# Kernel optimization log

Measured on AMD Instinct MI355X. Metric: run time of the kernel, lower is better.

Reference implementation:

```python
import jax, jax.numpy as jnp
import numpy as np

N, E = 50000, 800000
IN_CH, H, OUT_CH, ED, L = 64, 128, 128, 1, 4


def setup_inputs() -> dict:
    key = jax.random.key(0)
    ks = jax.random.split(key, 24)
    s = 0.02
    inp = {
        'h': jax.random.normal(ks[0], (N, IN_CH), jnp.float32),
        'coords': jax.random.normal(ks[1], (N, 3), jnp.float32),
        'edge_attr': jax.random.normal(ks[2], (E, ED), jnp.float32),
        'emb_in_W': jax.random.normal(ks[3], (IN_CH, H), jnp.float32) * s,
        'emb_in_b': jnp.zeros((H,), jnp.float32),
        'emb_out_W': jax.random.normal(ks[4], (H, OUT_CH), jnp.float32) * s,
        'emb_out_b': jnp.zeros((OUT_CH,), jnp.float32),
        # per-layer stacked params
        'eW1': jax.random.normal(ks[5], (L, 2 * H + 1 + ED, H), jnp.float32) * s,
        'eb1': jnp.zeros((L, H), jnp.float32),
        'eW2': jax.random.normal(ks[6], (L, H, H), jnp.float32) * s,
        'eb2': jnp.zeros((L, H), jnp.float32),
        'cW1': jax.random.normal(ks[7], (L, H, H), jnp.float32) * s,
        'cb1': jnp.zeros((L, H), jnp.float32),
        'cWc': jax.random.normal(ks[8], (L, H, 1), jnp.float32) * 0.001,  # xavier gain=0.001, no bias
        'nW1': jax.random.normal(ks[9], (L, 2 * H, H), jnp.float32) * s,
        'nb1': jnp.zeros((L, H), jnp.float32),
        'nW2': jax.random.normal(ks[10], (L, H, H), jnp.float32) * s,
        'nb2': jnp.zeros((L, H), jnp.float32),
        'edge_index': jax.random.randint(ks[11], (2, E), 0, N, jnp.int32),
    }
    return inp


def _egnn_forward(h, coords, edge_attr, emb_in_W, emb_in_b, emb_out_W, emb_out_b,
                  eW1, eb1, eW2, eb2, cW1, cb1, cWc, nW1, nb1, nW2, nb2, edge_index):
    silu = jax.nn.silu
    row, col = edge_index[0], edge_index[1]  # PyG: j=source=row, i=target=col
    # count of incoming edges per target node, for coords_agg='mean'
    counts = jax.ops.segment_sum(jnp.ones((E,), jnp.float32), col, num_segments=N)
    counts = jnp.maximum(counts, 1.0)[:, None]
    h = h @ emb_in_W + emb_in_b
    for l in range(L):
        coord_diff = coords[row] - coords[col]                       # [E,3]
        dist = jnp.sum(coord_diff * coord_diff, axis=-1, keepdims=True)  # [E,1]
        # message: edge MLP on cat(x_i, x_j, dist, edge_attr)
        edge_in = jnp.concatenate([h[col], h[row], dist, edge_attr], axis=-1)
        ef = silu(edge_in @ eW1[l] + eb1[l])
        ef = silu(ef @ eW2[l] + eb2[l])                               # [E,H]
        cw = silu(ef @ cW1[l] + cb1[l]) @ cWc[l]                      # [E,1]
        coord_upd = coord_diff * cw                                   # [E,3]
        # aggregate to target nodes
        agg_feat = jax.ops.segment_sum(ef, col, num_segments=N)       # [N,H]
        agg_coord = jax.ops.segment_sum(coord_upd, col, num_segments=N) / counts
        # node update (residual)
        node_in = jnp.concatenate([h, agg_feat], axis=-1)
        upd = silu(node_in @ nW1[l] + nb1[l]) @ nW2[l] + nb2[l]
        h = h + upd
        coords = coords + agg_coord
    h = h @ emb_out_W + emb_out_b
    return h, coords


def reference(h, coords, edge_attr, emb_in_W, emb_in_b, emb_out_W, emb_out_b,
              eW1, eb1, eW2, eb2, cW1, cb1, cWc, nW1, nb1, nW2, nb2, edge_index):
    return _egnn_forward(h, coords, edge_attr, emb_in_W, emb_in_b, emb_out_W, emb_out_b,
                         eW1, eb1, eW2, eb2, cW1, cb1, cWc, nW1, nb1, nW2, nb2, edge_index)
```

## Files before the change

kernel.cpp:

```cpp
#include <hip/hip_runtime.h>

constexpr int Nn = 50000;
constexpr int Ee = 800000;
constexpr int EF_STR  = 136;
constexpr int NIN_STR = 264;
constexpr int HIN_STR = 72;
constexpr int NB_SCAN = (Nn + 255) / 256;

typedef short s8v __attribute__((ext_vector_type(8)));
typedef float f4v __attribute__((ext_vector_type(4)));

__device__ __forceinline__ ushort f2bf(float f) {
    uint u = __float_as_uint(f);
    uint r = (u + 0x7FFFu + ((u >> 16) & 1u)) >> 16;
    return (ushort)r;
}
__device__ __forceinline__ ushort f2bf_t(float f) {
    return (ushort)(__float_as_uint(f) >> 16);
}
__device__ __forceinline__ float bf2f(ushort s) {
    return __uint_as_float(((uint)s) << 16);
}
__device__ __forceinline__ float silu_f(float x) {
    return x * __fdividef(1.0f, 1.0f + __expf(-x));
}
__device__ __forceinline__ uint pack2bf_t(float lo, float hi) {
    return __builtin_amdgcn_perm(__float_as_uint(hi), __float_as_uint(lo), 0x07060302u);
}
__device__ __forceinline__ uint pack2bf_r(float lo, float hi) {
    uint a = __float_as_uint(lo) + 0x8000u;
    uint b = __float_as_uint(hi) + 0x8000u;
    return __builtin_amdgcn_perm(b, a, 0x07060302u);
}

__device__ __forceinline__ void swz_one(const float* src, ushort* dst, int K, int lstride, int KC, int idx)
{
    int per = KC * 4096;
    int l = idx / per, r = idx % per;
    int fb = r >> 9, rem = r & 511;
    int lane = rem >> 3, jj = rem & 7;
    int kc = fb >> 3, t = fb & 7;
    int k = kc * 32 + ((lane >> 4) << 3) + jj;
    int n = t * 16 + (lane & 15);
    float v = (k < K) ? src[(size_t)l * lstride + (size_t)k * 128 + n] : 0.0f;
    dst[idx] = f2bf(v);
}
__global__ void __launch_bounds__(256) k_swz_all(
    const float* __restrict__ eW1, const float* __restrict__ eW2, const float* __restrict__ cW1,
    const float* __restrict__ nW1, const float* __restrict__ nW2,
    const float* __restrict__ inW, const float* __restrict__ outW,
    ushort* __restrict__ oT, ushort* __restrict__ oM,
    ushort* __restrict__ o2, ushort* __restrict__ o3,
    ushort* __restrict__ o4, ushort* __restrict__ o5,
    ushort* __restrict__ o6, ushort* __restrict__ o7)
{
    int gid = blockIdx.x * 256 + threadIdx.x;
    if (gid < 65536)       swz_one(eW1,         oT, 128, 33024, 4, gid);
    else if (gid < 131072) swz_one(eW1 + 16384, oM, 128, 33024, 4, gid - 65536);
    else if (gid < 196608) swz_one(eW2, o2, 128, 16384, 4, gid - 131072);
    else if (gid < 262144) swz_one(cW1, o3, 128, 16384, 4, gid - 196608);
    else if (gid < 393216) swz_one(nW1, o4, 256, 32768, 8, gid - 262144);
    else if (gid < 458752) swz_one(nW2, o5, 128, 16384, 4, gid - 393216);
    else if (gid < 466944) swz_one(inW, o6, 64, 8192, 2, gid - 458752);
    else if (gid < 483328) swz_one(outW, o7, 128, 16384, 4, gid - 466944);
}

__global__ void __launch_bounds__(256) k_count(const int* __restrict__ eidx, int* __restrict__ ecnt)
{
    int e = blockIdx.x * 256 + threadIdx.x;
    atomicAdd(&ecnt[eidx[Ee + e]], 1);
}

__global__ void __launch_bounds__(256) k_bsum(const int* __restrict__ ecnt, int* __restrict__ bsum)
{
    __shared__ int ws[4];
    int tid = threadIdx.x, lane = tid & 63, w = tid >> 6;
    int i = blockIdx.x * 256 + tid;
    int x = (i < Nn) ? ecnt[i] : 0;
    #pragma unroll
    for (int off = 1; off < 64; off <<= 1) x += __shfl_xor(x, off, 64);
    if (lane == 0) ws[w] = x;
    __syncthreads();
    if (tid == 0) bsum[blockIdx.x] = ws[0] + ws[1] + ws[2] + ws[3];
}
__global__ void __launch_bounds__(256) k_bscan(int* __restrict__ bsum)
{
    __shared__ int ws[4];
    int tid = threadIdx.x, lane = tid & 63, w = tid >> 6;
    int x = (tid < NB_SCAN) ? bsum[tid] : 0;
    int s = x;
    #pragma unroll
    for (int off = 1; off < 64; off <<= 1) {
        int t = __shfl_up(s, off, 64);
        if (lane >= off) s += t;
    }
    if (lane == 63) ws[w] = s;
    __syncthreads();
    if (tid == 0) { int a = 0; for (int k = 0; k < 4; k++) { int t = ws[k]; ws[k] = a; a += t; } }
    __syncthreads();
    int excl = ws[w] + s - x;
    if (tid < NB_SCAN) bsum[tid] = excl;
}
__global__ void __launch_bounds__(256) k_cursor(const int* __restrict__ ecnt,
                                               const int* __restrict__ boff, int* __restrict__ cursor)
{
    __shared__ int ws[4];
    int tid = threadIdx.x, lane = tid & 63, w = tid >> 6;
    int i = blockIdx.x * 256 + tid;
    int x = (i < Nn) ? ecnt[i] : 0;
    int s = x;
    #pragma unroll
    for (int off = 1; off < 64; off <<= 1) {
        int t = __shfl_up(s, off, 64);
        if (lane >= off) s += t;
    }
    if (lane == 63) ws[w] = s;
    __syncthreads();
    if (tid == 0) { int a = 0; for (int k = 0; k < 4; k++) { int t = ws[k]; ws[k] = a; a += t; } }
    __syncthreads();
    int excl = ws[w] + s - x + boff[blockIdx.x];
    if (i < Nn) cursor[i] = excl;
}

__global__ void __launch_bounds__(256) k_scatter(
    const int* __restrict__ eidx, const float* __restrict__ edge_attr,
    int* __restrict__ cursor,
    int* __restrict__ srow, int* __restrict__ scol, float* __restrict__ sattr)
{
    int e = blockIdx.x * 256 + threadIdx.x;
    int r = eidx[e], c = eidx[Ee + e];
    int p = atomicAdd(&cursor[c], 1);
    srow[p] = r; scol[p] = c; sattr[p] = edge_attr[e];
}

__global__ void __launch_bounds__(512, 2) k_emb(
    const float* __restrict__ h_in, const float* __restrict__ coords,
    const ushort* __restrict__ ws_, const float* __restrict__ b,
    float* __restrict__ hbuf, ushort* __restrict__ hbf, float* __restrict__ cbuf)
{
    __shared__ alignas(16) ushort s_h[64 * HIN_STR];
    const int tid = threadIdx.x;
    const int nb = blockIdx.x * 64;
    #pragma unroll
    for (int i = 0; i < 2; i++) {
        int idx = i * 512 + tid;
        int e = idx >> 4, ch = idx & 15;
        int node = nb + e;
        float4 f = make_float4(0.f, 0.f, 0.f, 0.f);
        if (node < Nn) f = *(const float4*)(h_in + (size_t)node * 64 + ch * 4);
        ushort4 u; u.x = f2bf(f.x); u.y = f2bf(f.y); u.z = f2bf(f.z); u.w = f2bf(f.w);
        *(ushort4*)(s_h + e * HIN_STR + ch * 4) = u;
    }
    if (tid < 192) {
        int n = nb + tid / 3, d = tid % 3;
        if (n < Nn) cbuf[n * 3 + d] = coords[n * 3 + d];
    }
    __syncthreads();
    const int lane = tid & 63, wave = tid >> 6;
    const int m = lane & 15, quad = lane >> 4;
    const int ws2 = wave >> 2, wt = wave & 3;
    const int rbase = ws2 * 32;
    f4v acc[2][2];
    #pragma unroll
    for (int nt = 0; nt < 2; nt++) { acc[nt][0] = (f4v){0,0,0,0}; acc[nt][1] = (f4v){0,0,0,0}; }
    const ushort* aBase = ws_ + wt * 1024 + lane * 8;
    #pragma unroll
    for (int kc = 0; kc < 2; kc++) {
        s8v a0 = *(const s8v*)(aBase + kc * 4096);
        s8v a1 = *(const s8v*)(aBase + kc * 4096 + 512);
        #pragma unroll
        for (int nt = 0; nt < 2; nt++) {
            s8v bf = *(const s8v*)(s_h + (rbase + nt * 16 + m) * HIN_STR + kc * 32 + quad * 8);
            acc[nt][0] = __builtin_amdgcn_mfma_f32_16x16x32_bf16(a0, bf, acc[nt][0], 0, 0, 0);
            acc[nt][1] = __builtin_amdgcn_mfma_f32_16x16x32_bf16(a1, bf, acc[nt][1], 0, 0, 0);
        }
    }
    #pragma unroll
    for (int nt = 0; nt < 2; nt++) {
        int node = nb + rbase + nt * 16 + m;
        if (node < Nn) {
            #pragma unroll
            for (int ct = 0; ct < 2; ct++) {
                int colb = (wt * 2 + ct) * 16 + quad * 4;
                float4 bb = *(const float4*)(b + colb);
                float v0 = acc[nt][ct][0] + bb.x;
                float v1 = acc[nt][ct][1] + bb.y;
                float v2 = acc[nt][ct][2] + bb.z;
                float v3 = acc[nt][ct][3] + bb.w;
                *(float4*)(hbuf + (size_t)node * 128 + colb) = make_float4(v0, v1, v2, v3);
                uint2 pk; pk.x = pack2bf_r(v0, v1); pk.y = pack2bf_r(v2, v3);
                *(uint2*)(hbf + (size_t)node * 128 + colb) = pk;
            }
        }
    }
}

__global__ void __launch_bounds__(512, 2) k_uv(
    const ushort* __restrict__ hbf,
    const ushort* __restrict__ topW, const ushort* __restrict__ midW,
    const float* __restrict__ b1, ushort* __restrict__ uvb)
{
    __shared__ alignas(16) ushort s_h[64 * EF_STR];
    const int tid = threadIdx.x;
    const int nb = blockIdx.x * 64;
    #pragma unroll
    for (int i = 0; i < 2; i++) {
        int idx = i * 512 + tid;
        int e = idx >> 4, ch = idx & 15;
        int node = nb + e;
        uint4 v = make_uint4(0, 0, 0, 0);
        if (node < Nn) v = *(const uint4*)(hbf + (size_t)node * 128 + ch * 8);
        *(uint4*)(s_h + e * EF_STR + ch * 8) = v;
    }
    __syncthreads();
    const int lane = tid & 63, wave = tid >> 6;
    const int m = lane & 15, quad = lane >> 4;
    const int ws2 = wave >> 2, wt = wave & 3;
    const int rbase = ws2 * 32;
    f4v au[2][2], av[2][2];
    #pragma unroll
    for (int ct = 0; ct < 2; ct++) {
        float4 bb = *(const float4*)(b1 + (wt * 2 + ct) * 16 + quad * 4);
        au[0][ct] = (f4v){bb.x, bb.y, bb.z, bb.w};
        au[1][ct] = au[0][ct];
        av[0][ct] = (f4v){0,0,0,0};
        av[1][ct] = (f4v){0,0,0,0};
    }
    const ushort* tBase = topW + wt * 1024 + (size_t)lane * 8;
    const ushort* mBase = midW + wt * 1024 + (size_t)lane * 8;
    #pragma unroll
    for (int kc = 0; kc < 4; kc++) {
        s8v t0 = *(const s8v*)(tBase + kc * 4096);
        s8v t1 = *(const s8v*)(tBase + kc * 4096 + 512);
        s8v m0 = *(const s8v*)(mBase + kc * 4096);
        s8v m1 = *(const s8v*)(mBase + kc * 4096 + 512);
        #pragma unroll
        for (int nt = 0; nt < 2; nt++) {
            s8v bf = *(const s8v*)(s_h + (rbase + nt * 16 + m) * EF_STR + kc * 32 + quad * 8);
            au[nt][0] = __builtin_amdgcn_mfma_f32_16x16x32_bf16(t0, bf, au[nt][0], 0, 0, 0);
            au[nt][1] = __builtin_amdgcn_mfma_f32_16x16x32_bf16(t1, bf, au[nt][1], 0, 0, 0);
            av[nt][0] = __builtin_amdgcn_mfma_f32_16x16x32_bf16(m0, bf, av[nt][0], 0, 0, 0);
            av[nt][1] = __builtin_amdgcn_mfma_f32_16x16x32_bf16(m1, bf, av[nt][1], 0, 0, 0);
        }
    }
    #pragma unroll
    for (int nt = 0; nt < 2; nt++) {
        int node = nb + rbase + nt * 16 + m;
        if (node < Nn) {
            #pragma unroll
            for (int ct = 0; ct < 2; ct++) {
                int colb = (wt * 2 + ct) * 16 + quad * 4;
                uint2 pu; pu.x = pack2bf_r(au[nt][ct][0], au[nt][ct][1]);
                          pu.y = pack2bf_r(au[nt][ct][2], au[nt][ct][3]);
                *(uint2*)(uvb + (size_t)node * 256 + colb) = pu;
                uint2 pv; pv.x = pack2bf_r(av[nt][ct][0], av[nt][ct][1]);
                          pv.y = pack2bf_r(av[nt][ct][2], av[nt][ct][3]);
                *(uint2*)(uvb + (size_t)node * 256 + 128 + colb) = pv;
            }
        }
    }
}

__global__ void __launch_bounds__(512, 8) k_edge(
    const float* __restrict__ cbuf,
    const int* __restrict__ srow, const int* __restrict__ scol, const float* __restrict__ sattr,
    const ushort* __restrict__ uvb,
    const float* __restrict__ wd, const float* __restrict__ wa,
    const ushort* __restrict__ w2s, const float* __restrict__ b2,
    const ushort* __restrict__ cw1s, const float* __restrict__ cb1,
    const float* __restrict__ cwc,
    float* __restrict__ agg_feat, float* __restrict__ agg_coord)
{
    __shared__ alignas(16) ushort s_a[64 * EF_STR];
    __shared__ alignas(16) ushort s_b[64 * EF_STR];
    __shared__ alignas(16) float  s_t[64 * 20];
    __shared__ int   s_col[64];
    __shared__ float s_cd[64 * 3];

    const int tid = threadIdx.x;
    const int eb = blockIdx.x * 64;

    if (tid < 64) {
        int rw = srow[eb + tid], cl = scol[eb + tid];
        s_col[tid] = cl;
        float d0 = cbuf[rw * 3 + 0] - cbuf[cl * 3 + 0];
        float d1 = cbuf[rw * 3 + 1] - cbuf[cl * 3 + 1];
        float d2 = cbuf[rw * 3 + 2] - cbuf[cl * 3 + 2];
        s_cd[tid * 3 + 0] = d0; s_cd[tid * 3 + 1] = d1; s_cd[tid * 3 + 2] = d2;
        s_t[tid * 20 + 16] = d0 * d0 + d1 * d1 + d2 * d2;
        s_t[tid * 20 + 17] = sattr[eb + tid];
        s_t[tid * 20 + 18] = __int_as_float(rw);
    }
    __syncthreads();

    {
        const int e = tid >> 3, ch = tid & 7;
        float dist = s_t[e * 20 + 16];
        float attr = s_t[e * 20 + 17];
        int row = __float_as_int(s_t[e * 20 + 18]);
        int col = s_col[e];
        const ushort* up = uvb + (size_t)col * 256 + ch * 16;
        const ushort* vp = uvb + (size_t)row * 256 + 128 + ch * 16;
        uint4 ua = *(const uint4*)up;
        uint4 ub = *(const uint4*)(up + 8);
        uint4 va = *(const uint4*)vp;
        uint4 vb = *(const uint4*)(vp + 8);
        float4 wdv[4], wav[4];
        #pragma unroll
        for (int i = 0; i < 4; i++) {
            wdv[i] = *(const float4*)(wd + ch * 16 + i * 4);
            wav[i] = *(const float4*)(wa + ch * 16 + i * 4);
        }
        const float* wdf = (const float*)wdv;
        const float* waf = (const float*)wav;
        uint uu[8] = {ua.x, ua.y, ua.z, ua.w, ub.x, ub.y, ub.z, ub.w};
        uint vv[8] = {va.x, va.y, va.z, va.w, vb.x, vb.y, vb.z, vb.w};
        uint pk[8];
        #pragma unroll
        for (int p = 0; p < 8; p++) {
            float ulo = __uint_as_float(uu[p] << 16);
            float uhi = __uint_as_float(uu[p] & 0xFFFF0000u);
            float vlo = __uint_as_float(vv[p] << 16);
            float vhi = __uint_as_float(vv[p] & 0xFFFF0000u);
            float lo = ulo + vlo + dist * wdf[2 * p] + attr * waf[2 * p];
            float hi = uhi + vhi + dist * wdf[2 * p + 1] + attr * waf[2 * p + 1];
            pk[p] = pack2bf_t(silu_f(lo), silu_f(hi));
        }
        *(uint4*)(s_a + e * EF_STR + ch * 16) = make_uint4(pk[0], pk[1], pk[2], pk[3]);
        *(uint4*)(s_a + e * EF_STR + ch * 16 + 8) = make_uint4(pk[4], pk[5], pk[6], pk[7]);
    }
    __syncthreads();

    const int lane = tid & 63, wave = tid >> 6;
    const int m = lane & 15, quad = lane >> 4;
    const int ws2 = wave >> 2, wt = wave & 3;
    const int rbase = ws2 * 32;

    {
        f4v acc2[2][2];
        float bias0 = b2[wt * 32 + m], bias1 = b2[wt * 32 + 16 + m];
        #pragma unroll
        for (int mt = 0; mt < 2; mt++) {
            acc2[mt][0] = (f4v){bias0, bias0, bias0, bias0};
            acc2[mt][1] = (f4v){bias1, bias1, bias1, bias1};
        }
        const ushort* bBase = w2s + wt * 1024 + (size_t)lane * 8;
        #pragma unroll
        for (int kc = 0; kc < 4; kc++) {
            s8v b0 = *(const s8v*)(bBase + kc * 4096);
            s8v b1v = *(const s8v*)(bBase + kc * 4096 + 512);
            #pragma unroll
            for (int mt = 0; mt < 2; mt++) {
                s8v a = *(const s8v*)(s_a + (rbase + mt * 16 + m) * EF_STR + kc * 32 + quad * 8);
                acc2[mt][0] = __builtin_amdgcn_mfma_f32_16x16x32_bf16(a, b0, acc2[mt][0], 0, 0, 0);
                acc2[mt][1] = __builtin_amdgcn_mfma_f32_16x16x32_bf16(a, b1v, acc2[mt][1], 0, 0, 0);
            }
        }
        #pragma unroll
        for (int tt = 0; tt < 2; tt++) {
            int col = (wt * 2 + tt) * 16 + m;
            #pragma unroll
            for (int mt = 0; mt < 2; mt++)
                #pragma unroll
                for (int r = 0; r < 4; r++)
                    s_b[(rbase + mt * 16 + quad * 4 + r) * EF_STR + col] = f2bf_t(silu_f(acc2[mt][tt][r]));
        }
    }
    __syncthreads();

    {
        f4v acc3[2][2];
        float bias0 = cb1[wt * 32 + m], bias1 = cb1[wt * 32 + 16 + m];
        float wc0 = cwc[wt * 32 + m],  wc1 = cwc[wt * 32 + 16 + m];
        #pragma unroll
        for (int mt = 0; mt < 2; mt++) {
            acc3[mt][0] = (f4v){bias0, bias0, bias0, bias0};
            acc3[mt][1] = (f4v){bias1, bias1, bias1, bias1};
        }
        const ushort* bBase = cw1s + wt * 1024 + (size_t)lane * 8;
        #pragma unroll
        for (int kc = 0; kc < 4; kc++) {
            s8v b0 = *(const s8v*)(bBase + kc * 4096);
            s8v b1v = *(const s8v*)(bBase + kc * 4096 + 512);
            #pragma unroll
            for (int mt = 0; mt < 2; mt++) {
                s8v a = *(const s8v*)(s_b + (rbase + mt * 16 + m) * EF_STR + kc * 32 + quad * 8);
                acc3[mt][0] = __builtin_amdgcn_mfma_f32_16x16x32_bf16(a, b0, acc3[mt][0], 0, 0, 0);
                acc3[mt][1] = __builtin_amdgcn_mfma_f32_16x16x32_bf16(a, b1v, acc3[mt][1], 0, 0, 0);
            }
        }
        #pragma unroll
        for (int mt = 0; mt < 2; mt++)
            #pragma unroll
            for (int r = 0; r < 4; r++) {
                float p = silu_f(acc3[mt][0][r]) * wc0 + silu_f(acc3[mt][1][r]) * wc1;
                p += __shfl_xor(p, 1, 64);
                p += __shfl_xor(p, 2, 64);
                if ((m & 3) == 0) {
                    int slot = wt * 4 + (m >> 2);
                    s_t[(rbase + mt * 16 + quad * 4 + r) * 20 + slot] = p;
                }
            }
    }
    __syncthreads();

    if (tid < 64) {
        float cw = 0.0f;
        #pragma unroll
        for (int l = 0; l < 16; l++) cw += s_t[tid * 20 + l];
        int cn = s_col[tid];
        unsafeAtomicAdd(&agg_coord[cn * 3 + 0], s_cd[tid * 3 + 0] * cw);
        unsafeAtomicAdd(&agg_coord[cn * 3 + 1], s_cd[tid * 3 + 1] * cw);
        unsafeAtomicAdd(&agg_coord[cn * 3 + 2], s_cd[tid * 3 + 2] * cw);
    }
    if (tid < 256) {
        int j = tid & 127;
        int e0 = (tid >> 7) * 32;
        float accv = 0.0f; int cur = s_col[e0];
        #pragma unroll 4
        for (int e = e0; e < e0 + 32; e++) {
            int c = s_col[e];
            if (c != cur) {
                unsafeAtomicAdd(&agg_feat[(size_t)cur * 128 + j], accv);
                accv = 0.0f; cur = c;
            }
            accv += bf2f(s_b[e * EF_STR + j]);
        }
        unsafeAtomicAdd(&agg_feat[(size_t)cur * 128 + j], accv);
    }
}

__global__ void __launch_bounds__(512, 6) k_node(
    float* __restrict__ hbuf, ushort* __restrict__ hbf, float* __restrict__ cbuf,
    float* __restrict__ agg_feat, float* __restrict__ agg_coord,
    const int* __restrict__ ecnt,
    const ushort* __restrict__ w1s, const float* __restrict__ b1,
    const ushort* __restrict__ w2s, const float* __restrict__ b2)
{
    __shared__ alignas(16) ushort s_nin[64 * NIN_STR];
    __shared__ alignas(16) ushort s_t1[64 * EF_STR];
    const int tid = threadIdx.x;
    const int nb = blockIdx.x * 64;

    #pragma unroll
    for (int i = 0; i < 2; i++) {
        int idx = i * 512 + tid;
        int e = idx >> 4, ch = idx & 15;
        int node = nb + e;
        uint4 v = make_uint4(0, 0, 0, 0);
        if (node < Nn) v = *(const uint4*)(hbf + (size_t)node * 128 + ch * 8);
        *(uint4*)(s_nin + e * NIN_STR + ch * 8) = v;
    }
    #pragma unroll
    for (int i = 0; i < 4; i++) {
        int idx = i * 512 + tid;
        int e = idx >> 5, ch = idx & 31;
        int node = nb + e;
        float4 f = make_float4(0.f, 0.f, 0.f, 0.f);
        if (node < Nn) {
            f = *(const float4*)(agg_feat + (size_t)node * 128 + ch * 4);
            *(float4*)(agg_feat + (size_t)node * 128 + ch * 4) = make_float4(0.f, 0.f, 0.f, 0.f);
        }
        uint2 pk; pk.x = pack2bf_t(f.x, f.y); pk.y = pack2bf_t(f.z, f.w);
        *(uint2*)(s_nin + e * NIN_STR + 128 + ch * 4) = pk;
    }
    if (tid < 64) {
        int n = nb + tid;
        if (n < Nn) {
            float c = (float)ecnt[n]; c = (c < 1.0f) ? 1.0f : c;
            float inv = __fdividef(1.0f, c);
            cbuf[n * 3 + 0] += agg_coord[n * 3 + 0] * inv;
            cbuf[n * 3 + 1] += agg_coord[n * 3 + 1] * inv;
            cbuf[n * 3 + 2] += agg_coord[n * 3 + 2] * inv;
            agg_coord[n * 3 + 0] = 0.f; agg_coord[n * 3 + 1] = 0.f; agg_coord[n * 3 + 2] = 0.f;
        }
    }
    __syncthreads();

    const int lane = tid & 63, wave = tid >> 6;
    const int m = lane & 15, quad = lane >> 4;
    const int ws2 = wave >> 2, wt = wave & 3;
    const int rbase = ws2 * 32;

    {
        f4v acc[2][2];
        #pragma unroll
        for (int ct = 0; ct < 2; ct++) {
            float4 bb = *(const float4*)(b1 + (wt * 2 + ct) * 16 + quad * 4);
            acc[0][ct] = (f4v){bb.x, bb.y, bb.z, bb.w};
            acc[1][ct] = acc[0][ct];
        }
        const ushort* aBase = w1s + wt * 1024 + (size_t)lane * 8;
        #pragma unroll
        for (int kc = 0; kc < 8; kc++) {
            s8v a0 = *(const s8v*)(aBase + kc * 4096);
            s8v a1 = *(const s8v*)(aBase + kc * 4096 + 512);
            #pragma unroll
            for (int nt = 0; nt < 2; nt++) {
                s8v bf = *(const s8v*)(s_nin + (rbase + nt * 16 + m) * NIN_STR + kc * 32 + quad * 8);
                acc[nt][0] = __builtin_amdgcn_mfma_f32_16x16x32_bf16(a0, bf, acc[nt][0], 0, 0, 0);
                acc[nt][1] = __builtin_amdgcn_mfma_f32_16x16x32_bf16(a1, bf, acc[nt][1], 0, 0, 0);
            }
        }
        #pragma unroll
        for (int nt = 0; nt < 2; nt++) {
            int row = rbase + nt * 16 + m;
            #pragma unroll
            for (int ct = 0; ct < 2; ct++) {
                int colb = (wt * 2 + ct) * 16 + quad * 4;
                float v0 = silu_f(acc[nt][ct][0]);
                float v1 = silu_f(acc[nt][ct][1]);
                float v2 = silu_f(acc[nt][ct][2]);
                float v3 = silu_f(acc[nt][ct][3]);
                uint2 pk; pk.x = pack2bf_t(v0, v1); pk.y = pack2bf_t(v2, v3);
                *(uint2*)(s_t1 + row * EF_STR + colb) = pk;
            }
        }
    }
    __syncthreads();

    {
        f4v acc[2][2];
        #pragma unroll
        for (int ct = 0; ct < 2; ct++) {
            float4 bb = *(const float4*)(b2 + (wt * 2 + ct) * 16 + quad * 4);
            acc[0][ct] = (f4v){bb.x, bb.y, bb.z, bb.w};
            acc[1][ct] = acc[0][ct];
        }
        const ushort* aBase = w2s + wt * 1024 + (size_t)lane * 8;
        #pragma unroll
        for (int kc = 0; kc < 4; kc++) {
            s8v a0 = *(const s8v*)(aBase + kc * 4096);
            s8v a1 = *(const s8v*)(aBase + kc * 4096 + 512);
            #pragma unroll
            for (int nt = 0; nt < 2; nt++) {
                s8v bf = *(const s8v*)(s_t1 + (rbase + nt * 16 + m) * EF_STR + kc * 32 + quad * 8);
                acc[nt][0] = __builtin_amdgcn_mfma_f32_16x16x32_bf16(a0, bf, acc[nt][0], 0, 0, 0);
                acc[nt][1] = __builtin_amdgcn_mfma_f32_16x16x32_bf16(a1, bf, acc[nt][1], 0, 0, 0);
            }
        }
        #pragma unroll
        for (int nt = 0; nt < 2; nt++) {
            int node = nb + rbase + nt * 16 + m;
            if (node < Nn) {
                #pragma unroll
                for (int ct = 0; ct < 2; ct++) {
                    int colb = (wt * 2 + ct) * 16 + quad * 4;
                    float4 old = *(const float4*)(hbuf + (size_t)node * 128 + colb);
                    float v0 = old.x + acc[nt][ct][0];
                    float v1 = old.y + acc[nt][ct][1];
                    float v2 = old.z + acc[nt][ct][2];
                    float v3 = old.w + acc[nt][ct][3];
                    *(float4*)(hbuf + (size_t)node * 128 + colb) = make_float4(v0, v1, v2, v3);
                    uint2 pk; pk.x = pack2bf_r(v0, v1); pk.y = pack2bf_r(v2, v3);
                    *(uint2*)(hbf + (size_t)node * 128 + colb) = pk;
                }
            }
        }
    }
}

__global__ void __launch_bounds__(512, 2) k_emb_out(
    const ushort* __restrict__ hbf, const float* __restrict__ cbuf,
    const ushort* __restrict__ ws_, const float* __restrict__ b, float* __restrict__ out)
{
    __shared__ alignas(16) ushort s_h[64 * EF_STR];
    const int tid = threadIdx.x;
    const int nb = blockIdx.x * 64;
    #pragma unroll
    for (int i = 0; i < 2; i++) {
        int idx = i * 512 + tid;
        int e = idx >> 4, ch = idx & 15;
        int node = nb + e;
        uint4 v = make_uint4(0, 0, 0, 0);
        if (node < Nn) v = *(const uint4*)(hbf + (size_t)node * 128 + ch * 8);
        *(uint4*)(s_h + e * EF_STR + ch * 8) = v;
    }
    if (tid < 192) {
        int n = nb + tid / 3, d = tid % 3;
        if (n < Nn) out[(size_t)Nn * 128 + n * 3 + d] = cbuf[n * 3 + d];
    }
    __syncthreads();
    const int lane = tid & 63, wave = tid >> 6;
    const int m = lane & 15, quad = lane >> 4;
    const int ws2 = wave >> 2, wt = wave & 3;
    const int rbase = ws2 * 32;
    f4v acc[2][2];
    #pragma unroll
    for (int ct = 0; ct < 2; ct++) {
        float4 bb = *(const float4*)(b + (wt * 2 + ct) * 16 + quad * 4);
        acc[0][ct] = (f4v){bb.x, bb.y, bb.z, bb.w};
        acc[1][ct] = acc[0][ct];
    }
    const ushort* aBase = ws_ + wt * 1024 + (size_t)lane * 8;
    #pragma unroll
    for (int kc = 0; kc < 4; kc++) {
        s8v a0 = *(const s8v*)(aBase + kc * 4096);
        s8v a1 = *(const s8v*)(aBase + kc * 4096 + 512);
        #pragma unroll
        for (int nt = 0; nt < 2; nt++) {
            s8v bf = *(const s8v*)(s_h + (rbase + nt * 16 + m) * EF_STR + kc * 32 + quad * 8);
            acc[nt][0] = __builtin_amdgcn_mfma_f32_16x16x32_bf16(a0, bf, acc[nt][0], 0, 0, 0);
            acc[nt][1] = __builtin_amdgcn_mfma_f32_16x16x32_bf16(a1, bf, acc[nt][1], 0, 0, 0);
        }
    }
    #pragma unroll
    for (int nt = 0; nt < 2; nt++) {
        int node = nb + rbase + nt * 16 + m;
        if (node < Nn) {
            #pragma unroll
            for (int ct = 0; ct < 2; ct++) {
                int colb = (wt * 2 + ct) * 16 + quad * 4;
                float4 o = make_float4(acc[nt][ct][0], acc[nt][ct][1],
                                       acc[nt][ct][2], acc[nt][ct][3]);
                *(float4*)(out + (size_t)node * 128 + colb) = o;
            }
        }
    }
}

extern "C" void kernel_launch(void* const* d_in, const int* in_sizes, int n_in,
                              void* d_out, int out_size, void* d_ws, size_t ws_size,
                              hipStream_t stream)
{
    const float* h_in      = (const float*)d_in[0];
    const float* coords    = (const float*)d_in[1];
    const float* edge_attr = (const float*)d_in[2];
    const float* emb_in_W  = (const float*)d_in[3];
    const float* emb_in_b  = (const float*)d_in[4];
    const float* emb_out_W = (const float*)d_in[5];
    const float* emb_out_b = (const float*)d_in[6];
    const float* eW1 = (const float*)d_in[7];
    const float* eb1 = (const float*)d_in[8];
    const float* eW2 = (const float*)d_in[9];
    const float* eb2 = (const float*)d_in[10];
    const float* cW1 = (const float*)d_in[11];
    const float* cb1 = (const float*)d_in[12];
    const float* cWc = (const float*)d_in[13];
    const float* nW1 = (const float*)d_in[14];
    const float* nb1 = (const float*)d_in[15];
    const float* nW2 = (const float*)d_in[16];
    const float* nb2 = (const float*)d_in[17];
    const int*  eidx = (const int*)d_in[18];

    size_t off = 0;
    char* base = (char*)d_ws;
    auto alloc = [&](size_t bytes) -> char* {
        char* p = base + off;
        off += (bytes + 255) & ~(size_t)255;
        return p;
    };
    float*  hbuf      = (float*)alloc((size_t)Nn * 128 * 4);
    ushort* hbf       = (ushort*)alloc((size_t)Nn * 128 * 2);
    ushort* uvb       = (ushort*)alloc((size_t)Nn * 256 * 2);
    float*  cbuf      = (float*)alloc((size_t)Nn * 3 * 4);
    int*    ecnt      = (int*)alloc((size_t)Nn * 4);
    int*    cursor    = (int*)alloc((size_t)Nn * 4);
    int*    bsum      = (int*)alloc((size_t)NB_SCAN * 4);
    int*    srow      = (int*)alloc((size_t)Ee * 4);
    int*    scol      = (int*)alloc((size_t)Ee * 4);
    float*  sattr     = (float*)alloc((size_t)Ee * 4);
    float*  agg_feat  = (float*)alloc((size_t)Nn * 128 * 4);
    float*  agg_coord = (float*)alloc((size_t)Nn * 3 * 4);
    ushort* eW1tops   = (ushort*)alloc((size_t)4 * 16384 * 2);
    ushort* eW1mids   = (ushort*)alloc((size_t)4 * 16384 * 2);
    ushort* eW2s      = (ushort*)alloc((size_t)4 * 16384 * 2);
    ushort* cW1s      = (ushort*)alloc((size_t)4 * 16384 * 2);
    ushort* nW1s      = (ushort*)alloc((size_t)4 * 32768 * 2);
    ushort* nW2s      = (ushort*)alloc((size_t)4 * 16384 * 2);
    ushort* eInWs     = (ushort*)alloc((size_t)8192 * 2);
    ushort* eOutWs    = (ushort*)alloc((size_t)16384 * 2);

    k_swz_all<<<483328 / 256, 256, 0, stream>>>(
        eW1, eW2, cW1, nW1, nW2, emb_in_W, emb_out_W,
        eW1tops, eW1mids, eW2s, cW1s, nW1s, nW2s, eInWs, eOutWs);

    hipMemsetAsync(ecnt, 0, (size_t)Nn * 4, stream);
    k_count<<<Ee / 256, 256, 0, stream>>>(eidx, ecnt);
    k_bsum<<<NB_SCAN, 256, 0, stream>>>(ecnt, bsum);
    k_bscan<<<1, 256, 0, stream>>>(bsum);
    k_cursor<<<NB_SCAN, 256, 0, stream>>>(ecnt, bsum, cursor);
    k_scatter<<<Ee / 256, 256, 0, stream>>>(eidx, edge_attr, cursor, srow, scol, sattr);
    k_emb<<<(Nn + 63) / 64, 512, 0, stream>>>(h_in, coords, eInWs, emb_in_b, hbuf, hbf, cbuf);

    hipMemsetAsync(agg_feat, 0, (size_t)Nn * 128 * 4, stream);
    hipMemsetAsync(agg_coord, 0, (size_t)Nn * 3 * 4, stream);

    for (int l = 0; l < 4; l++) {
        k_uv<<<(Nn + 63) / 64, 512, 0, stream>>>(
            hbf, eW1tops + (size_t)l * 16384, eW1mids + (size_t)l * 16384,
            eb1 + l * 128, uvb);
        k_edge<<<Ee / 64, 512, 0, stream>>>(
            cbuf, srow, scol, sattr, uvb,
            eW1 + ((size_t)l * 258 + 256) * 128,
            eW1 + ((size_t)l * 258 + 257) * 128,
            eW2s + (size_t)l * 16384, eb2 + l * 128,
            cW1s + (size_t)l * 16384, cb1 + l * 128,
            cWc + l * 128,
            agg_feat, agg_coord);
        k_node<<<(Nn + 63) / 64, 512, 0, stream>>>(
            hbuf, hbf, cbuf, agg_feat, agg_coord, ecnt,
            nW1s + (size_t)l * 32768, nb1 + l * 128,
            nW2s + (size_t)l * 16384, nb2 + l * 128);
    }
    k_emb_out<<<(Nn + 63) / 64, 512, 0, stream>>>(hbf, cbuf, eOutWs, emb_out_b, (float*)d_out);
}
```

Before: 1.643 ms.

## Hoist edge gathers before sync, transpose MFMA operands, widen aggregation threads

Each thread now loads its edge's row/col indices, attribute and the gathered bf16 U/V node projections before the first barrier, so the global gathers overlap the coordinate-difference work. The MFMA operand order is swapped so each lane holds four consecutive output columns of one edge row. This allows packed uint2 LDS stores and a cross-quad shuffle reduction of the coordinate weight into four partial slots instead of sixteen. The feature aggregation now uses all 512 threads over 16-edge segments instead of 256 threads over 32, which can issue more atomics when target columns repeat.

```diff
diff --git a/kernel.cpp b/kernel.cpp
--- a/kernel.cpp
+++ b/kernel.cpp
@@ -261,6 +261,18 @@
     }
 }
 
+__device__ __forceinline__ uint uv_term(uint uw, uint vw, float dist, float attr,
+                                        const float* wdp, const float* wap, int j)
+{
+    float2 w2d = *(const float2*)(wdp + 2 * j);
+    float2 w2a = *(const float2*)(wap + 2 * j);
+    float lo = __uint_as_float(uw << 16) + __uint_as_float(vw << 16)
+             + dist * w2d.x + attr * w2a.x;
+    float hi = __uint_as_float(uw & 0xFFFF0000u) + __uint_as_float(vw & 0xFFFF0000u)
+             + dist * w2d.y + attr * w2a.y;
+    return pack2bf_t(silu_f(lo), silu_f(hi));
+}
+
 __global__ void __launch_bounds__(512, 8) k_edge(
     const float* __restrict__ cbuf,
     const int* __restrict__ srow, const int* __restrict__ scol, const float* __restrict__ sattr,
@@ -280,6 +292,17 @@
     const int tid = threadIdx.x;
     const int eb = blockIdx.x * 64;
 
+    const int e = tid >> 3, ch = tid & 7;
+    const int myrow = srow[eb + e];
+    const int mycol = scol[eb + e];
+    const float attr = sattr[eb + e];
+    const ushort* up = uvb + (size_t)mycol * 256 + ch * 16;
+    const ushort* vp = uvb + (size_t)myrow * 256 + 128 + ch * 16;
+    uint4 ua = *(const uint4*)up;
+    uint4 ub = *(const uint4*)(up + 8);
+    uint4 va = *(const uint4*)vp;
+    uint4 vb = *(const uint4*)(vp + 8);
+
     if (tid < 64) {
         int rw = srow[eb + tid], cl = scol[eb + tid];
         s_col[tid] = cl;
@@ -288,46 +311,24 @@
         float d2 = cbuf[rw * 3 + 2] - cbuf[cl * 3 + 2];
         s_cd[tid * 3 + 0] = d0; s_cd[tid * 3 + 1] = d1; s_cd[tid * 3 + 2] = d2;
         s_t[tid * 20 + 16] = d0 * d0 + d1 * d1 + d2 * d2;
-        s_t[tid * 20 + 17] = sattr[eb + tid];
-        s_t[tid * 20 + 18] = __int_as_float(rw);
     }
     __syncthreads();
 
     {
-        const int e = tid >> 3, ch = tid & 7;
-        float dist = s_t[e * 20 + 16];
-        float attr = s_t[e * 20 + 17];
-        int row = __float_as_int(s_t[e * 20 + 18]);
-        int col = s_col[e];
-        const ushort* up = uvb + (size_t)col * 256 + ch * 16;
-        const ushort* vp = uvb + (size_t)row * 256 + 128 + ch * 16;
-        uint4 ua = *(const uint4*)up;
-        uint4 ub = *(const uint4*)(up + 8);
-        uint4 va = *(const uint4*)vp;
-        uint4 vb = *(const uint4*)(vp + 8);
-        float4 wdv[4], wav[4];
-        #pragma unroll
-        for (int i = 0; i < 4; i++) {
-            wdv[i] = *(const float4*)(wd + ch * 16 + i * 4);
-            wav[i] = *(const float4*)(wa + ch * 16 + i * 4);
-        }
-        const float* wdf = (const float*)wdv;
-        const float* waf = (const float*)wav;
-        uint uu[8] = {ua.x, ua.y, ua.z, ua.w, ub.x, ub.y, ub.z, ub.w};
-        uint vv[8] = {va.x, va.y, va.z, va.w, vb.x, vb.y, vb.z, vb.w};
-        uint pk[8];
-        #pragma unroll
-        for (int p = 0; p < 8; p++) {
-            float ulo = __uint_as_float(uu[p] << 16);
-            float uhi = __uint_as_float(uu[p] & 0xFFFF0000u);
-            float vlo = __uint_as_float(vv[p] << 16);
-            float vhi = __uint_as_float(vv[p] & 0xFFFF0000u);
-            float lo = ulo + vlo + dist * wdf[2 * p] + attr * waf[2 * p];
-            float hi = uhi + vhi + dist * wdf[2 * p + 1] + attr * waf[2 * p + 1];
-            pk[p] = pack2bf_t(silu_f(lo), silu_f(hi));
-        }
-        *(uint4*)(s_a + e * EF_STR + ch * 16) = make_uint4(pk[0], pk[1], pk[2], pk[3]);
-        *(uint4*)(s_a + e * EF_STR + ch * 16 + 8) = make_uint4(pk[4], pk[5], pk[6], pk[7]);
+        const float dist = s_t[e * 20 + 16];
+        const float* wdp = wd + ch * 16;
+        const float* wap = wa + ch * 16;
+        uint4 q0, q1;
+        q0.x = uv_term(ua.x, va.x, dist, attr, wdp, wap, 0);
+        q0.y = uv_term(ua.y, va.y, dist, attr, wdp, wap, 1);
+        q0.z = uv_term(ua.z, va.z, dist, attr, wdp, wap, 2);
+        q0.w = uv_term(ua.w, va.w, dist, attr, wdp, wap, 3);
+        *(uint4*)(s_a + e * EF_STR + ch * 16) = q0;
+        q1.x = uv_term(ub.x, vb.x, dist, attr, wdp, wap, 4);
+        q1.y = uv_term(ub.y, vb.y, dist, attr, wdp, wap, 5);
+        q1.z = uv_term(ub.z, vb.z, dist, attr, wdp, wap, 6);
+        q1.w = uv_term(ub.w, vb.w, dist, attr, wdp, wap, 7);
+        *(uint4*)(s_a + e * EF_STR + ch * 16 + 8) = q1;
     }
     __syncthreads();
 
@@ -338,11 +339,11 @@
 
     {
         f4v acc2[2][2];
-        float bias0 = b2[wt * 32 + m], bias1 = b2[wt * 32 + 16 + m];
-        #pragma unroll
-        for (int mt = 0; mt < 2; mt++) {
-            acc2[mt][0] = (f4v){bias0, bias0, bias0, bias0};
-            acc2[mt][1] = (f4v){bias1, bias1, bias1, bias1};
+        #pragma unroll
+        for (int tt = 0; tt < 2; tt++) {
+            float4 bb = *(const float4*)(b2 + (wt * 2 + tt) * 16 + quad * 4);
+            acc2[0][tt] = (f4v){bb.x, bb.y, bb.z, bb.w};
+            acc2[1][tt] = acc2[0][tt];
         }
         const ushort* bBase = w2s + wt * 1024 + (size_t)lane * 8;
         #pragma unroll
@@ -352,30 +353,29 @@
             #pragma unroll
             for (int mt = 0; mt < 2; mt++) {
                 s8v a = *(const s8v*)(s_a + (rbase + mt * 16 + m) * EF_STR + kc * 32 + quad * 8);
-                acc2[mt][0] = __builtin_amdgcn_mfma_f32_16x16x32_bf16(a, b0, acc2[mt][0], 0, 0, 0);
-                acc2[mt][1] = __builtin_amdgcn_mfma_f32_16x16x32_bf16(a, b1v, acc2[mt][1], 0, 0, 0);
-            }
-        }
-        #pragma unroll
-        for (int tt = 0; tt < 2; tt++) {
-            int col = (wt * 2 + tt) * 16 + m;
-            #pragma unroll
-            for (int mt = 0; mt < 2; mt++)
-                #pragma unroll
-                for (int r = 0; r < 4; r++)
-                    s_b[(rbase + mt * 16 + quad * 4 + r) * EF_STR + col] = f2bf_t(silu_f(acc2[mt][tt][r]));
-        }
+                acc2[mt][0] = __builtin_amdgcn_mfma_f32_16x16x32_bf16(b0, a, acc2[mt][0], 0, 0, 0);
+                acc2[mt][1] = __builtin_amdgcn_mfma_f32_16x16x32_bf16(b1v, a, acc2[mt][1], 0, 0, 0);
+            }
+        }
+        #pragma unroll
+        for (int mt = 0; mt < 2; mt++)
+            #pragma unroll
+            for (int tt = 0; tt < 2; tt++) {
+                uint2 pk;
+                pk.x = pack2bf_t(silu_f(acc2[mt][tt][0]), silu_f(acc2[mt][tt][1]));
+                pk.y = pack2bf_t(silu_f(acc2[mt][tt][2]), silu_f(acc2[mt][tt][3]));
+                *(uint2*)(s_b + (rbase + mt * 16 + m) * EF_STR + (wt * 2 + tt) * 16 + quad * 4) = pk;
+            }
     }
     __syncthreads();
 
     {
         f4v acc3[2][2];
-        float bias0 = cb1[wt * 32 + m], bias1 = cb1[wt * 32 + 16 + m];
-        float wc0 = cwc[wt * 32 + m],  wc1 = cwc[wt * 32 + 16 + m];
-        #pragma unroll
-        for (int mt = 0; mt < 2; mt++) {
-            acc3[mt][0] = (f4v){bias0, bias0, bias0, bias0};
-            acc3[mt][1] = (f4v){bias1, bias1, bias1, bias1};
+        #pragma unroll
+        for (int tt = 0; tt < 2; tt++) {
+            float4 bb = *(const float4*)(cb1 + (wt * 2 + tt) * 16 + quad * 4);
+            acc3[0][tt] = (f4v){bb.x, bb.y, bb.z, bb.w};
+            acc3[1][tt] = acc3[0][tt];
         }
         const ushort* bBase = cw1s + wt * 1024 + (size_t)lane * 8;
         #pragma unroll
@@ -385,46 +385,49 @@
             #pragma unroll
             for (int mt = 0; mt < 2; mt++) {
                 s8v a = *(const s8v*)(s_b + (rbase + mt * 16 + m) * EF_STR + kc * 32 + quad * 8);
-                acc3[mt][0] = __builtin_amdgcn_mfma_f32_16x16x32_bf16(a, b0, acc3[mt][0], 0, 0, 0);
-                acc3[mt][1] = __builtin_amdgcn_mfma_f32_16x16x32_bf16(a, b1v, acc3[mt][1], 0, 0, 0);
-            }
-        }
-        #pragma unroll
-        for (int mt = 0; mt < 2; mt++)
-            #pragma unroll
-            for (int r = 0; r < 4; r++) {
-                float p = silu_f(acc3[mt][0][r]) * wc0 + silu_f(acc3[mt][1][r]) * wc1;
-                p += __shfl_xor(p, 1, 64);
-                p += __shfl_xor(p, 2, 64);
-                if ((m & 3) == 0) {
-                    int slot = wt * 4 + (m >> 2);
-                    s_t[(rbase + mt * 16 + quad * 4 + r) * 20 + slot] = p;
-                }
-            }
+                acc3[mt][0] = __builtin_amdgcn_mfma_f32_16x16x32_bf16(b0, a, acc3[mt][0], 0, 0, 0);
+                acc3[mt][1] = __builtin_amdgcn_mfma_f32_16x16x32_bf16(b1v, a, acc3[mt][1], 0, 0, 0);
+            }
+        }
+        float p0 = 0.0f, p1 = 0.0f;
+        #pragma unroll
+        for (int tt = 0; tt < 2; tt++) {
+            float4 wc = *(const float4*)(cwc + (wt * 2 + tt) * 16 + quad * 4);
+            p0 += silu_f(acc3[0][tt][0]) * wc.x + silu_f(acc3[0][tt][1]) * wc.y
+                + silu_f(acc3[0][tt][2]) * wc.z + silu_f(acc3[0][tt][3]) * wc.w;
+            p1 += silu_f(acc3[1][tt][0]) * wc.x + silu_f(acc3[1][tt][1]) * wc.y
+                + silu_f(acc3[1][tt][2]) * wc.z + silu_f(acc3[1][tt][3]) * wc.w;
+        }
+        p0 += __shfl_xor(p0, 16, 64);
+        p0 += __shfl_xor(p0, 32, 64);
+        p1 += __shfl_xor(p1, 16, 64);
+        p1 += __shfl_xor(p1, 32, 64);
+        if (quad == 0) {
+            s_t[(rbase + m) * 20 + wt] = p0;
+            s_t[(rbase + 16 + m) * 20 + wt] = p1;
+        }
     }
     __syncthreads();
 
     if (tid < 64) {
-        float cw = 0.0f;
-        #pragma unroll
-        for (int l = 0; l < 16; l++) cw += s_t[tid * 20 + l];
+        float cw = s_t[tid * 20 + 0] + s_t[tid * 20 + 1] + s_t[tid * 20 + 2] + s_t[tid * 20 + 3];
         int cn = s_col[tid];
         unsafeAtomicAdd(&agg_coord[cn * 3 + 0], s_cd[tid * 3 + 0] * cw);
         unsafeAtomicAdd(&agg_coord[cn * 3 + 1], s_cd[tid * 3 + 1] * cw);
         unsafeAtomicAdd(&agg_coord[cn * 3 + 2], s_cd[tid * 3 + 2] * cw);
     }
-    if (tid < 256) {
+    {
         int j = tid & 127;
-        int e0 = (tid >> 7) * 32;
+        int e0 = (tid >> 7) * 16;
         float accv = 0.0f; int cur = s_col[e0];
         #pragma unroll 4
-        for (int e = e0; e < e0 + 32; e++) {
-            int c = s_col[e];
+        for (int ee = e0; ee < e0 + 16; ee++) {
+            int c = s_col[ee];
             if (c != cur) {
                 unsafeAtomicAdd(&agg_feat[(size_t)cur * 128 + j], accv);
                 accv = 0.0f; cur = c;
             }
-            accv += bf2f(s_b[e * EF_STR + j]);
+            accv += bf2f(s_b[ee * EF_STR + j]);
         }
         unsafeAtomicAdd(&agg_feat[(size_t)cur * 128 + j], accv);
     }
```

Result: no change. 1.642 ms (-0.1%).
